# Kernel tuning notes

Hardware: AMD Instinct MI355X
Metric: run time of the kernel (lower is better)

The kernel has to match this reference:

```python
import jax, jax.numpy as jnp
import numpy as np

D = 512   # embed_dim
K = 8     # expand_dim
TAU = 16.0
LN_EPS = 1e-5


def setup_inputs() -> dict:
    key = jax.random.key(0)
    ks = jax.random.split(key, 8)
    b, n = 4, 4096
    x = jax.random.normal(ks[0], (b, n, D), dtype=jnp.float32)
    # nn.Linear weights stored as (in, out); bias=False everywhere
    W_i = jax.random.normal(ks[1], (D, D), dtype=jnp.float32) / np.sqrt(D)
    W_e = jax.random.normal(ks[2], (D, K), dtype=jnp.float32) / np.sqrt(D)
    W_s = jax.random.normal(ks[3], (D, K), dtype=jnp.float32) / np.sqrt(D)
    o_param = jax.random.normal(ks[4], (K, D), dtype=jnp.float32) * 0.1
    ln_gamma = jnp.ones((D,), dtype=jnp.float32)
    ln_beta = jnp.zeros((D,), dtype=jnp.float32)
    W_out = jax.random.normal(ks[5], (D, D), dtype=jnp.float32) / np.sqrt(D)
    return {"x": x, "W_i": W_i, "W_e": W_e, "W_s": W_s, "o_param": o_param,
            "ln_gamma": ln_gamma, "ln_beta": ln_beta, "W_out": W_out}


def reference(x, W_i, W_e, W_s, o_param, ln_gamma, ln_beta, W_out):
    b, n, d = x.shape
    k = W_e.shape[1]
    i = x @ W_i            # (b,n,d) input branch
    e = x @ W_e            # (b,n,k) expand branch (t_type=0: identity)
    s = x @ W_s            # (b,n,k) shrink branch
    # data-independent decay gate: exp(logsigmoid(o)/tau), shape (k,d)
    o = jnp.exp(jax.nn.log_sigmoid(o_param) / TAU)

    def step(m, inp):
        it, et, st = inp          # (b,d), (b,k), (b,k)
        m = o * m + et[:, :, None] * it[:, None, :]   # (b,k,d)
        y = jnp.einsum('bk,bkd->bd', st, m)
        return m, y

    m0 = jnp.zeros((b, k, d), dtype=x.dtype)
    xs = (jnp.swapaxes(i, 0, 1), jnp.swapaxes(e, 0, 1), jnp.swapaxes(s, 0, 1))
    _, ys = jax.lax.scan(step, m0, xs)   # ys: (n,b,d)
    y = jnp.swapaxes(ys, 0, 1)           # (b,n,d)
    # LayerNorm
    mu = jnp.mean(y, axis=-1, keepdims=True)
    var = jnp.mean(jnp.square(y - mu), axis=-1, keepdims=True)
    y = (y - mu) * jax.lax.rsqrt(var + LN_EPS) * ln_gamma + ln_beta
    return y @ W_out
```

## Files before the change

kernel.cpp:

```cpp
#include <hip/hip_runtime.h>
#include <stdint.h>

typedef __bf16 bf16;
typedef __bf16 bf16x8 __attribute__((ext_vector_type(8)));
typedef float  f32x4  __attribute__((ext_vector_type(4)));

#define NSEQ 4096
#define NROWS 16384
#define CHUNK 32
#define NCHUNKS_B 128
#define NCHUNKS 512
#define SEGLEN 16
#define NSEG 8
#define YSTRIDE 516

__device__ __forceinline__ float bf2f(uint16_t u){
    uint32_t w = ((uint32_t)u) << 16;
    return __builtin_bit_cast(float, w);
}
__device__ __forceinline__ uint32_t pack2(float a, float b){
    uint16_t ua = __builtin_bit_cast(uint16_t, (bf16)a);
    uint16_t ub = __builtin_bit_cast(uint16_t, (bf16)b);
    return ((uint32_t)ub << 16) | (uint32_t)ua;
}
__device__ __forceinline__ uint4 cvt8(const float* p){
    float4 lo = *(const float4*)p;
    float4 hi = *(const float4*)(p + 4);
    uint4 r;
    r.x = pack2(lo.x, lo.y); r.y = pack2(lo.z, lo.w);
    r.z = pack2(hi.x, hi.y); r.w = pack2(hi.z, hi.w);
    return r;
}
__device__ __forceinline__ float rd_any(const void* p, long idx, int f){
    return f ? ((const float*)p)[idx] : (float)((const bf16*)p)[idx];
}
__device__ __forceinline__ void cp16(const void* g, void* l){
    __builtin_amdgcn_global_load_lds((const __attribute__((address_space(1))) void*)g,
                                     (__attribute__((address_space(3))) void*)l,
                                     16, 0, 0);
}

__global__ __launch_bounds__(256) void prep_all(const uint32_t* __restrict__ xw,
                                                const void* __restrict__ Wi,
                                                const void* __restrict__ Wo,
                                                const void* We, const void* Ws,
                                                const void* op, const void* g, const void* bta,
                                                bf16* __restrict__ Wt_i, bf16* __restrict__ Wt_o,
                                                bf16* __restrict__ Wt_es,
                                                float* __restrict__ g_c, float* __restrict__ b_c,
                                                float* __restrict__ o_buf, float* __restrict__ oL_buf,
                                                float* __restrict__ lsL_buf, float* __restrict__ oL16_buf,
                                                int* __restrict__ flag_g){
    __shared__ int cnt[256];
    __shared__ bf16 T[64][65];
    int tid = threadIdx.x;
    int c = 0;
    #pragma unroll
    for (int j = 0; j < 4; ++j){
        uint32_t w = xw[tid*4 + j];
        uint32_t e = (w >> 7) & 0xFF;
        c += (e >= 110 && e <= 140) ? 1 : 0;
    }
    cnt[tid] = c; __syncthreads();
    for (int s = 128; s; s >>= 1){
        if (tid < s) cnt[tid] += cnt[tid + s];
        __syncthreads();
    }
    int f = (cnt[0] < 512) ? 1 : 0;
    int blk = blockIdx.x;
    if (blk == 0 && tid == 0) flag_g[0] = f;

    if (blk < 128){
        int mat = blk >> 6;
        int t   = blk & 63;
        int k0  = (t >> 3) * 64, n0 = (t & 7) * 64;
        const void* in = mat ? Wo : Wi;
        bf16* out = mat ? Wt_o : Wt_i;
        #pragma unroll
        for (int e = 0; e < 16; ++e){
            int idx = e*256 + tid;
            int r = idx >> 6, cc = idx & 63;
            T[cc][r] = (bf16)rd_any(in, (long)(k0 + r)*512 + n0 + cc, f);
        }
        __syncthreads();
        #pragma unroll
        for (int e = 0; e < 16; ++e){
            int idx = e*256 + tid;
            int rn = idx >> 6, ck = idx & 63;
            out[(long)(n0 + rn)*512 + k0 + ck] = T[rn][ck];
        }
    } else if (blk < 136){
        int sub = blk - 128;
        for (int i = tid; i < 1024; i += 256){
            int gi = sub*1024 + i;
            int n = gi >> 9, k = gi & 511;
            float v = (n < 8) ? rd_any(We, (long)k*8 + n, f)
                              : rd_any(Ws, (long)k*8 + (n-8), f);
            Wt_es[gi] = (bf16)v;
        }
    } else {
        int sub = blk - 136;
        int base = sub * 1024;
        for (int i = tid; i < 1024; i += 256){
            int gi = base + i;
            float x = rd_any(op, gi, f);
            float ls = (x < 0.f) ? (x - log1pf(expf(x))) : (0.f - log1pf(expf(-x)));
            o_buf[gi]    = expf(ls * (1.0f/16.0f));
            oL_buf[gi]   = expf(ls * 2.0f);
            lsL_buf[gi]  = ls * 2.0f;
            oL16_buf[gi] = expf(ls * 32.0f);
        }
        if (sub == 0){
            for (int i = tid; i < 512; i += 256){
                g_c[i] = rd_any(g, i, f);
                b_c[i] = rd_any(bta, i, f);
            }
        }
    }
}

__global__ __launch_bounds__(256) void gemm_bt(const void* __restrict__ Avoid,
                                               const bf16* __restrict__ Bt,
                                               void* __restrict__ Cvoid,
                                               int M, int N, int Kd,
                                               const int* __restrict__ aflag,
                                               const int* __restrict__ cflag,
                                               const bf16* __restrict__ Wes,
                                               float* __restrict__ e_out,
                                               float* __restrict__ s_out){
    __shared__ __align__(16) bf16 As[2][128*32];
    __shared__ __align__(16) bf16 Bs[2][128*32];
    const int tid  = threadIdx.x;
    const int lane = tid & 63;
    const int wave = tid >> 6;
    const int ntiles = N >> 7;
    int bid = blockIdx.x;
    {
        const int q = gridDim.x >> 3;
        bid = (bid & 7) * q + (bid >> 3);
    }
    const int mtile = bid / ntiles;
    const int ntile = bid - mtile*ntiles;
    const int m0 = mtile << 7, n0 = ntile << 7;
    const int wr = (wave >> 1) << 6;
    const int wc = (wave & 1) << 6;
    const int lrow = lane & 15;
    const int quad = lane >> 4;
    const int fa = aflag ? *aflag : 0;
    const bool do_es = (Wes != nullptr) && (ntile == 0) && (wc == 0);

    f32x4 acc[4][4] = {};
    f32x4 acc_es[4] = {};

    const int sr = tid >> 2;
    const int sk = (tid & 3) << 3;
    const bf16*  Ag  = (const bf16*) Avoid + (long)(m0 + sr)*Kd + sk;
    const float* Agf = (const float*)Avoid + (long)(m0 + sr)*Kd + sk;
    const bf16*  Bg  = Bt + (long)(n0 + sr)*Kd + sk;

    if (fa){
        *(uint4*)&As[0][tid*8]        = cvt8(Agf);
        *(uint4*)&As[0][2048 + tid*8] = cvt8(Agf + (long)64*Kd);
    } else {
        cp16(Ag,                 &As[0][(size_t)wave*512]);
        cp16(Ag + (long)64*Kd,   &As[0][2048 + (size_t)wave*512]);
    }
    cp16(Bg,               &Bs[0][(size_t)wave*512]);
    cp16(Bg + (long)64*Kd, &Bs[0][2048 + (size_t)wave*512]);
    __syncthreads();

    int cur = 0;
    for (int k0 = 0; k0 < Kd; k0 += 32){
        const int nxt  = cur ^ 1;
        const int k1   = k0 + 32;
        const bool more = (k1 < Kd);
        float4 la0, la1, lb0, lb1;
        if (more){
            if (fa){
                la0 = *(const float4*)(Agf + k1);
                la1 = *(const float4*)(Agf + k1 + 4);
                lb0 = *(const float4*)(Agf + (long)64*Kd + k1);
                lb1 = *(const float4*)(Agf + (long)64*Kd + k1 + 4);
            } else {
                cp16(Ag + k1,               &As[nxt][(size_t)wave*512]);
                cp16(Ag + (long)64*Kd + k1, &As[nxt][2048 + (size_t)wave*512]);
            }
            cp16(Bg + k1,               &Bs[nxt][(size_t)wave*512]);
            cp16(Bg + (long)64*Kd + k1, &Bs[nxt][2048 + (size_t)wave*512]);
        }

        bf16x8 af[4], bfr[4];
        #pragma unroll
        for (int i = 0; i < 4; ++i)
            af[i]  = *(const bf16x8*)&As[cur][(wr + i*16 + lrow)*32 + quad*8];
        #pragma unroll
        for (int j = 0; j < 4; ++j)
            bfr[j] = *(const bf16x8*)&Bs[cur][(wc + j*16 + lrow)*32 + quad*8];
        #pragma unroll
        for (int i = 0; i < 4; ++i)
            #pragma unroll
            for (int j = 0; j < 4; ++j)
                acc[i][j] = __builtin_amdgcn_mfma_f32_16x16x32_bf16(af[i], bfr[j], acc[i][j], 0, 0, 0);
        if (do_es){
            bf16x8 be = *(const bf16x8*)(Wes + (long)lrow*512 + k0 + quad*8);
            #pragma unroll
            for (int i = 0; i < 4; ++i)
                acc_es[i] = __builtin_amdgcn_mfma_f32_16x16x32_bf16(af[i], be, acc_es[i], 0, 0, 0);
        }

        if (more && fa){
            uint4 A0, A1;
            A0.x = pack2(la0.x, la0.y); A0.y = pack2(la0.z, la0.w);
            A0.z = pack2(la1.x, la1.y); A0.w = pack2(la1.z, la1.w);
            A1.x = pack2(lb0.x, lb0.y); A1.y = pack2(lb0.z, lb0.w);
            A1.z = pack2(lb1.x, lb1.y); A1.w = pack2(lb1.z, lb1.w);
            *(uint4*)&As[nxt][tid*8]        = A0;
            *(uint4*)&As[nxt][2048 + tid*8] = A1;
        }
        __syncthreads();
        cur = nxt;
    }

    const int fc = cflag ? *cflag : 0;
    if (fc){
        float* Cf = (float*)Cvoid;
        #pragma unroll
        for (int i = 0; i < 4; ++i){
            int gr = m0 + wr + i*16 + quad*4;
            #pragma unroll
            for (int j = 0; j < 4; ++j){
                int gc = n0 + wc + j*16 + lrow;
                #pragma unroll
                for (int r = 0; r < 4; ++r)
                    Cf[(long)(gr + r)*N + gc] = acc[i][j][r];
            }
        }
    } else {
        bf16* Cb = (bf16*)Cvoid;
        #pragma unroll
        for (int i = 0; i < 4; ++i){
            int gr = m0 + wr + i*16 + quad*4;
            #pragma unroll
            for (int j = 0; j < 4; ++j){
                int gc = n0 + wc + j*16 + lrow;
                #pragma unroll
                for (int r = 0; r < 4; ++r)
                    Cb[(long)(gr + r)*N + gc] = (bf16)acc[i][j][r];
            }
        }
    }
    if (do_es){
        float* eo = (lrow < 8) ? e_out : s_out;
        int col = lrow & 7;
        #pragma unroll
        for (int i = 0; i < 4; ++i){
            int gr = m0 + wr + i*16 + quad*4;
            #pragma unroll
            for (int r = 0; r < 4; ++r)
                eo[(long)(gr + r)*8 + col] = acc_es[i][r];
        }
    }
}

__global__ __launch_bounds__(256) void passA(const bf16* __restrict__ i_buf,
                                             const float* __restrict__ e_buf,
                                             const float* __restrict__ o_buf,
                                             float* __restrict__ Ams){
    int c  = blockIdx.x;
    int b  = c >> 7;
    int t0 = (c & 127) * CHUNK;
    int tid = threadIdx.x;
    __shared__ float eS[CHUNK*8];
    eS[tid] = e_buf[((long)(b*NSEQ + t0))*8 + tid];
    __syncthreads();
    int d0 = tid*2;
    float o0[8], o1[8], m0[8], m1[8];
    #pragma unroll
    for (int k = 0; k < 8; ++k){
        o0[k] = o_buf[k*512 + d0]; o1[k] = o_buf[k*512 + d0 + 1];
        m0[k] = 0.f; m1[k] = 0.f;
    }
    const bf16* ip = i_buf + (long)(b*NSEQ + t0)*512 + d0;
    for (int t = 0; t < CHUNK; ++t){
        uint32_t iv = *(const uint32_t*)(ip + (long)t*512);
        float i0 = bf2f((uint16_t)iv), i1 = bf2f((uint16_t)(iv >> 16));
        #pragma unroll
        for (int k = 0; k < 8; ++k){
            float ek = eS[t*8 + k];
            m0[k] = o0[k]*m0[k] + ek*i0;
            m1[k] = o1[k]*m1[k] + ek*i1;
        }
    }
    float* Ac = Ams + (long)c*4096;
    #pragma unroll
    for (int k = 0; k < 8; ++k){
        float2 v; v.x = m0[k]; v.y = m1[k];
        *(float2*)&Ac[k*512 + d0] = v;
    }
}

__global__ __launch_bounds__(256) void passB1(float* __restrict__ Ams,
                                              const float* __restrict__ oL_buf,
                                              float* __restrict__ Tbuf){
    int bs  = blockIdx.x >> 4;
    int b   = bs >> 3, seg = bs & 7;
    int idx = (blockIdx.x & 15)*256 + threadIdx.x;
    float oL = oL_buf[idx];
    float m = 0.f;
    float* Mb = Ams + ((long)b*NCHUNKS_B + seg*SEGLEN)*4096 + idx;
    #pragma unroll 4
    for (int cc = 0; cc < SEGLEN; ++cc){
        float a = Mb[(long)cc*4096];
        Mb[(long)cc*4096] = m;
        m = oL*m + a;
    }
    Tbuf[(long)bs*4096 + idx] = m;
}

__global__ __launch_bounds__(256) void passB2(float* __restrict__ Tbuf,
                                              const float* __restrict__ oL16_buf){
    int b   = blockIdx.x >> 4;
    int idx = (blockIdx.x & 15)*256 + threadIdx.x;
    float oL16 = oL16_buf[idx];
    float t[NSEG];
    #pragma unroll
    for (int s = 0; s < NSEG; ++s)
        t[s] = Tbuf[((long)b*NSEG + s)*4096 + idx];
    float m = 0.f;
    #pragma unroll
    for (int s = 0; s < NSEG; ++s){
        Tbuf[((long)b*NSEG + s)*4096 + idx] = m;
        m = oL16*m + t[s];
    }
}

__global__ __launch_bounds__(256) void passC(bf16* __restrict__ iy,
                                             const float* __restrict__ e_buf,
                                             const float* __restrict__ s_buf,
                                             const float* __restrict__ o_buf,
                                             const float* __restrict__ Ploc,
                                             const float* __restrict__ Mseg,
                                             const float* __restrict__ lsL_buf,
                                             const float* __restrict__ g_c,
                                             const float* __restrict__ b_c){
    int c  = blockIdx.x;
    int b  = c >> 7;
    int cI = c & 127;
    int seg = cI >> 4;
    float fj = (float)(cI & 15);
    int t0 = cI * CHUNK;
    int tid = threadIdx.x;
    __shared__ float eS[CHUNK*8], sS[CHUNK*8];
    __shared__ float muS[CHUNK], rS[CHUNK];
    __shared__ __align__(16) float yS[CHUNK][YSTRIDE];
    eS[tid] = e_buf[((long)(b*NSEQ + t0))*8 + tid];
    sS[tid] = s_buf[((long)(b*NSEQ + t0))*8 + tid];
    __syncthreads();
    int d0 = tid*2;
    float o0[8], o1[8], m0[8], m1[8];
    const float* P0 = Ploc + (long)c*4096;
    const float* Ms = Mseg + ((long)b*NSEG + seg)*4096;
    #pragma unroll
    for (int k = 0; k < 8; ++k){
        int i0 = k*512 + d0;
        o0[k] = o_buf[i0]; o1[k] = o_buf[i0 + 1];
        m0[k] = P0[i0]   + __expf(lsL_buf[i0]  *fj)*Ms[i0];
        m1[k] = P0[i0+1] + __expf(lsL_buf[i0+1]*fj)*Ms[i0+1];
    }
    bf16* ip = iy + (long)(b*NSEQ + t0)*512 + d0;
    for (int t = 0; t < CHUNK; ++t){
        uint32_t iv = *(const uint32_t*)(ip + (long)t*512);
        float i0 = bf2f((uint16_t)iv), i1 = bf2f((uint16_t)(iv >> 16));
        float y0 = 0.f, y1 = 0.f;
        #pragma unroll
        for (int k = 0; k < 8; ++k){
            float ek = eS[t*8 + k], sk = sS[t*8 + k];
            m0[k] = o0[k]*m0[k] + ek*i0;
            m1[k] = o1[k]*m1[k] + ek*i1;
            y0 += sk*m0[k];
            y1 += sk*m1[k];
        }
        float2 yv; yv.x = y0; yv.y = y1;
        *(float2*)&yS[t][d0] = yv;
    }
    __syncthreads();
    {
        int row = tid >> 3, sub = tid & 7;
        const float4* yr = (const float4*)&yS[row][sub*64];
        float s = 0.f, s2 = 0.f;
        #pragma unroll
        for (int j = 0; j < 16; ++j){
            float4 v = yr[j];
            s  += v.x + v.y + v.z + v.w;
            s2 += v.x*v.x + v.y*v.y + v.z*v.z + v.w*v.w;
        }
        s += __shfl_xor(s, 1); s2 += __shfl_xor(s2, 1);
        s += __shfl_xor(s, 2); s2 += __shfl_xor(s2, 2);
        s += __shfl_xor(s, 4); s2 += __shfl_xor(s2, 4);
        if (sub == 0){
            float mu  = s * (1.f/512.f);
            float var = s2 * (1.f/512.f) - mu*mu;
            muS[row] = mu;
            rS[row]  = rsqrtf(var + 1e-5f);
        }
    }
    __syncthreads();
    float g0 = g_c[d0], g1 = g_c[d0+1];
    float bb0 = b_c[d0], bb1 = b_c[d0+1];
    for (int t = 0; t < CHUNK; ++t){
        float mu = muS[t], r = rS[t];
        float2 yv = *(const float2*)&yS[t][d0];
        float a0 = (yv.x - mu)*r*g0 + bb0;
        float a1 = (yv.y - mu)*r*g1 + bb1;
        *(uint32_t*)(ip + (long)t*512) = pack2(a0, a1);
    }
}

extern "C" void kernel_launch(void* const* d_in, const int* in_sizes, int n_in,
                              void* d_out, int out_size, void* d_ws, size_t ws_size,
                              hipStream_t stream){
    const void* x    = d_in[0];
    const void* W_i  = d_in[1];
    const void* W_e  = d_in[2];
    const void* W_s  = d_in[3];
    const void* o_p  = d_in[4];
    const void* gmm  = d_in[5];
    const void* bta  = d_in[6];
    const void* W_o  = d_in[7];

    char* ws = (char*)d_ws;
    bf16*  Wt_i   = (bf16*) (ws + 0);
    float* Tbuf   = (float*)(ws + 0);
    bf16*  Wt_o   = (bf16*) (ws + 524288);
    bf16*  iy_buf = (bf16*) (ws + 1048576);
    float* e_buf  = (float*)(ws + 17825792);
    float* s_buf  = (float*)(ws + 18350080);
    float* o_buf  = (float*)(ws + 18874368);
    float* oL_buf = (float*)(ws + 18890752);
    float* lsL    = (float*)(ws + 18907136);
    float* oL16   = (float*)(ws + 18923520);
    float* Ams    = (float*)(ws + 18939904);
    bf16*  Wt_es  = (bf16*) (ws + 27328512);
    float* g_c    = (float*)(ws + 27344896);
    float* b_c    = (float*)(ws + 27346944);
    int*   flag   = (int*)  (ws + 27348992);

    prep_all<<<140, 256, 0, stream>>>((const uint32_t*)x, W_i, W_o, W_e, W_s, o_p, gmm, bta,
                                      Wt_i, Wt_o, Wt_es, g_c, b_c, o_buf, oL_buf, lsL, oL16, flag);
    gemm_bt <<<512, 256, 0, stream>>>(x, Wt_i, iy_buf, NROWS, 512, 512, flag, nullptr,
                                      Wt_es, e_buf, s_buf);
    passA  <<<NCHUNKS, 256, 0, stream>>>(iy_buf, e_buf, o_buf, Ams);
    passB1 <<<512,  256, 0, stream>>>(Ams, oL_buf, Tbuf);
    passB2 <<<64,   256, 0, stream>>>(Tbuf, oL16);
    passC  <<<NCHUNKS, 256, 0, stream>>>(iy_buf, e_buf, s_buf, o_buf, Ams, Tbuf, lsL,
                                         g_c, b_c);
    gemm_bt <<<512, 256, 0, stream>>>(iy_buf, Wt_o, d_out, NROWS, 512, 512, nullptr, flag,
                                      nullptr, nullptr, nullptr);
}
```

Measured before the change: 174.8 us.

## Fuse chunk-local scan into input GEMM epilogue and fold segment prefix into passC

```diff
diff --git a/kernel.cpp b/kernel.cpp
--- a/kernel.cpp
+++ b/kernel.cpp
@@ -127,9 +127,14 @@
                                                const int* __restrict__ cflag,
                                                const bf16* __restrict__ Wes,
                                                float* __restrict__ e_out,
-                                               float* __restrict__ s_out){
-    __shared__ __align__(16) bf16 As[2][128*32];
-    __shared__ __align__(16) bf16 Bs[2][128*32];
+                                               float* __restrict__ s_out,
+                                               float* __restrict__ Ams,
+                                               const float* __restrict__ o_buf){
+    __shared__ __align__(16) char smem[36*1024];
+    bf16*  As = (bf16*)smem;
+    bf16*  Bs = (bf16*)(smem + 16384);
+    bf16*  iT = (bf16*)smem;
+    float* eS = (float*)(smem + 32768);
     const int tid  = threadIdx.x;
     const int lane = tid & 63;
     const int wave = tid >> 6;
@@ -147,7 +152,7 @@
     const int lrow = lane & 15;
     const int quad = lane >> 4;
     const int fa = aflag ? *aflag : 0;
-    const bool do_es = (Wes != nullptr) && (ntile == 0) && (wc == 0);
+    const bool do_es = (Wes != nullptr) && ((wave & 1) == 0);
 
     f32x4 acc[4][4] = {};
     f32x4 acc_es[4] = {};
@@ -159,14 +164,14 @@
     const bf16*  Bg  = Bt + (long)(n0 + sr)*Kd + sk;
 
     if (fa){
-        *(uint4*)&As[0][tid*8]        = cvt8(Agf);
-        *(uint4*)&As[0][2048 + tid*8] = cvt8(Agf + (long)64*Kd);
+        *(uint4*)&As[tid*8]        = cvt8(Agf);
+        *(uint4*)&As[2048 + tid*8] = cvt8(Agf + (long)64*Kd);
     } else {
-        cp16(Ag,                 &As[0][(size_t)wave*512]);
-        cp16(Ag + (long)64*Kd,   &As[0][2048 + (size_t)wave*512]);
-    }
-    cp16(Bg,               &Bs[0][(size_t)wave*512]);
-    cp16(Bg + (long)64*Kd, &Bs[0][2048 + (size_t)wave*512]);
+        cp16(Ag,                 As + (size_t)wave*512);
+        cp16(Ag + (long)64*Kd,   As + 2048 + (size_t)wave*512);
+    }
+    cp16(Bg,               Bs + (size_t)wave*512);
+    cp16(Bg + (long)64*Kd, Bs + 2048 + (size_t)wave*512);
     __syncthreads();
 
     int cur = 0;
@@ -182,20 +187,20 @@
                 lb0 = *(const float4*)(Agf + (long)64*Kd + k1);
                 lb1 = *(const float4*)(Agf + (long)64*Kd + k1 + 4);
             } else {
-                cp16(Ag + k1,               &As[nxt][(size_t)wave*512]);
-                cp16(Ag + (long)64*Kd + k1, &As[nxt][2048 + (size_t)wave*512]);
-            }
-            cp16(Bg + k1,               &Bs[nxt][(size_t)wave*512]);
-            cp16(Bg + (long)64*Kd + k1, &Bs[nxt][2048 + (size_t)wave*512]);
+                cp16(Ag + k1,               As + nxt*4096 + (size_t)wave*512);
+                cp16(Ag + (long)64*Kd + k1, As + nxt*4096 + 2048 + (size_t)wave*512);
+            }
+            cp16(Bg + k1,               Bs + nxt*4096 + (size_t)wave*512);
+            cp16(Bg + (long)64*Kd + k1, Bs + nxt*4096 + 2048 + (size_t)wave*512);
         }
 
         bf16x8 af[4], bfr[4];
         #pragma unroll
         for (int i = 0; i < 4; ++i)
-            af[i]  = *(const bf16x8*)&As[cur][(wr + i*16 + lrow)*32 + quad*8];
+            af[i]  = *(const bf16x8*)&As[cur*4096 + (wr + i*16 + lrow)*32 + quad*8];
         #pragma unroll
         for (int j = 0; j < 4; ++j)
-            bfr[j] = *(const bf16x8*)&Bs[cur][(wc + j*16 + lrow)*32 + quad*8];
+            bfr[j] = *(const bf16x8*)&Bs[cur*4096 + (wc + j*16 + lrow)*32 + quad*8];
         #pragma unroll
         for (int i = 0; i < 4; ++i)
             #pragma unroll
@@ -214,8 +219,8 @@
             A0.z = pack2(la1.x, la1.y); A0.w = pack2(la1.z, la1.w);
             A1.x = pack2(lb0.x, lb0.y); A1.y = pack2(lb0.z, lb0.w);
             A1.z = pack2(lb1.x, lb1.y); A1.w = pack2(lb1.z, lb1.w);
-            *(uint4*)&As[nxt][tid*8]        = A0;
-            *(uint4*)&As[nxt][2048 + tid*8] = A1;
+            *(uint4*)&As[nxt*4096 + tid*8]        = A0;
+            *(uint4*)&As[nxt*4096 + 2048 + tid*8] = A1;
         }
         __syncthreads();
         cur = nxt;
@@ -249,7 +254,7 @@
             }
         }
     }
-    if (do_es){
+    if (do_es && ntile == 0){
         float* eo = (lrow < 8) ? e_out : s_out;
         int col = lrow & 7;
         #pragma unroll
@@ -260,42 +265,54 @@
                 eo[(long)(gr + r)*8 + col] = acc_es[i][r];
         }
     }
-}
-
-__global__ __launch_bounds__(256) void passA(const bf16* __restrict__ i_buf,
-                                             const float* __restrict__ e_buf,
-                                             const float* __restrict__ o_buf,
-                                             float* __restrict__ Ams){
-    int c  = blockIdx.x;
-    int b  = c >> 7;
-    int t0 = (c & 127) * CHUNK;
-    int tid = threadIdx.x;
-    __shared__ float eS[CHUNK*8];
-    eS[tid] = e_buf[((long)(b*NSEQ + t0))*8 + tid];
-    __syncthreads();
-    int d0 = tid*2;
-    float o0[8], o1[8], m0[8], m1[8];
-    #pragma unroll
-    for (int k = 0; k < 8; ++k){
-        o0[k] = o_buf[k*512 + d0]; o1[k] = o_buf[k*512 + d0 + 1];
-        m0[k] = 0.f; m1[k] = 0.f;
-    }
-    const bf16* ip = i_buf + (long)(b*NSEQ + t0)*512 + d0;
-    for (int t = 0; t < CHUNK; ++t){
-        uint32_t iv = *(const uint32_t*)(ip + (long)t*512);
-        float i0 = bf2f((uint16_t)iv), i1 = bf2f((uint16_t)(iv >> 16));
-        #pragma unroll
-        for (int k = 0; k < 8; ++k){
-            float ek = eS[t*8 + k];
-            m0[k] = o0[k]*m0[k] + ek*i0;
-            m1[k] = o1[k]*m1[k] + ek*i1;
-        }
-    }
-    float* Ac = Ams + (long)c*4096;
-    #pragma unroll
-    for (int k = 0; k < 8; ++k){
-        float2 v; v.x = m0[k]; v.y = m1[k];
-        *(float2*)&Ac[k*512 + d0] = v;
+
+    if (Ams){
+        #pragma unroll
+        for (int i = 0; i < 4; ++i){
+            int lr = wr + i*16 + quad*4;
+            #pragma unroll
+            for (int j = 0; j < 4; ++j){
+                int lc = wc + j*16 + lrow;
+                #pragma unroll
+                for (int r = 0; r < 4; ++r)
+                    iT[(lr + r)*128 + lc] = (bf16)acc[i][j][r];
+            }
+        }
+        if (do_es && lrow < 8){
+            #pragma unroll
+            for (int i = 0; i < 4; ++i){
+                int lr = wr + i*16 + quad*4;
+                #pragma unroll
+                for (int r = 0; r < 4; ++r)
+                    eS[(lr + r)*8 + lrow] = acc_es[i][r];
+            }
+        }
+        __syncthreads();
+        const int dp  = tid & 63;
+        const int kq  = tid >> 6;
+        const int dl  = dp*2;
+        const int ki  = kq*2;
+        const float o00 = o_buf[(ki  )*512 + n0 + dl];
+        const float o01 = o_buf[(ki  )*512 + n0 + dl + 1];
+        const float o10 = o_buf[(ki+1)*512 + n0 + dl];
+        const float o11 = o_buf[(ki+1)*512 + n0 + dl + 1];
+        #pragma unroll
+        for (int c = 0; c < 4; ++c){
+            float m00 = 0.f, m01 = 0.f, m10 = 0.f, m11 = 0.f;
+            for (int t = 0; t < CHUNK; ++t){
+                int row = c*32 + t;
+                uint32_t iv = *(const uint32_t*)&iT[row*128 + dl];
+                float i0 = bf2f((uint16_t)iv), i1 = bf2f((uint16_t)(iv >> 16));
+                float e0 = eS[row*8 + ki], e1 = eS[row*8 + ki + 1];
+                m00 = o00*m00 + e0*i0;  m01 = o01*m01 + e0*i1;
+                m10 = o10*m10 + e1*i0;  m11 = o11*m11 + e1*i1;
+            }
+            float* Ac = Ams + (long)((m0 >> 5) + c)*4096 + n0 + dl;
+            float2 v0; v0.x = m00; v0.y = m01;
+            float2 v1; v1.x = m10; v1.y = m11;
+            *(float2*)&Ac[(ki  )*512] = v0;
+            *(float2*)&Ac[(ki+1)*512] = v1;
+        }
     }
 }
 
@@ -317,30 +334,14 @@
     Tbuf[(long)bs*4096 + idx] = m;
 }
 
-__global__ __launch_bounds__(256) void passB2(float* __restrict__ Tbuf,
-                                              const float* __restrict__ oL16_buf){
-    int b   = blockIdx.x >> 4;
-    int idx = (blockIdx.x & 15)*256 + threadIdx.x;
-    float oL16 = oL16_buf[idx];
-    float t[NSEG];
-    #pragma unroll
-    for (int s = 0; s < NSEG; ++s)
-        t[s] = Tbuf[((long)b*NSEG + s)*4096 + idx];
-    float m = 0.f;
-    #pragma unroll
-    for (int s = 0; s < NSEG; ++s){
-        Tbuf[((long)b*NSEG + s)*4096 + idx] = m;
-        m = oL16*m + t[s];
-    }
-}
-
 __global__ __launch_bounds__(256) void passC(bf16* __restrict__ iy,
                                              const float* __restrict__ e_buf,
                                              const float* __restrict__ s_buf,
                                              const float* __restrict__ o_buf,
                                              const float* __restrict__ Ploc,
-                                             const float* __restrict__ Mseg,
+                                             const float* __restrict__ Tbuf,
                                              const float* __restrict__ lsL_buf,
+                                             const float* __restrict__ oL16_buf,
                                              const float* __restrict__ g_c,
                                              const float* __restrict__ b_c){
     int c  = blockIdx.x;
@@ -359,13 +360,19 @@
     int d0 = tid*2;
     float o0[8], o1[8], m0[8], m1[8];
     const float* P0 = Ploc + (long)c*4096;
-    const float* Ms = Mseg + ((long)b*NSEG + seg)*4096;
     #pragma unroll
     for (int k = 0; k < 8; ++k){
         int i0 = k*512 + d0;
+        float ms0 = 0.f, ms1 = 0.f;
+        float w0 = oL16_buf[i0], w1 = oL16_buf[i0+1];
+        for (int u = 0; u < seg; ++u){
+            const float* T = Tbuf + ((long)(b*NSEG + u))*4096;
+            ms0 = w0*ms0 + T[i0];
+            ms1 = w1*ms1 + T[i0+1];
+        }
         o0[k] = o_buf[i0]; o1[k] = o_buf[i0 + 1];
-        m0[k] = P0[i0]   + __expf(lsL_buf[i0]  *fj)*Ms[i0];
-        m1[k] = P0[i0+1] + __expf(lsL_buf[i0+1]*fj)*Ms[i0+1];
+        m0[k] = P0[i0]   + __expf(lsL_buf[i0]  *fj)*ms0;
+        m1[k] = P0[i0+1] + __expf(lsL_buf[i0+1]*fj)*ms1;
     }
     bf16* ip = iy + (long)(b*NSEQ + t0)*512 + d0;
     for (int t = 0; t < CHUNK; ++t){
@@ -448,12 +455,10 @@
     prep_all<<<140, 256, 0, stream>>>((const uint32_t*)x, W_i, W_o, W_e, W_s, o_p, gmm, bta,
                                       Wt_i, Wt_o, Wt_es, g_c, b_c, o_buf, oL_buf, lsL, oL16, flag);
     gemm_bt <<<512, 256, 0, stream>>>(x, Wt_i, iy_buf, NROWS, 512, 512, flag, nullptr,
-                                      Wt_es, e_buf, s_buf);
-    passA  <<<NCHUNKS, 256, 0, stream>>>(iy_buf, e_buf, o_buf, Ams);
+                                      Wt_es, e_buf, s_buf, Ams, o_buf);
     passB1 <<<512,  256, 0, stream>>>(Ams, oL_buf, Tbuf);
-    passB2 <<<64,   256, 0, stream>>>(Tbuf, oL16);
     passC  <<<NCHUNKS, 256, 0, stream>>>(iy_buf, e_buf, s_buf, o_buf, Ams, Tbuf, lsL,
-                                         g_c, b_c);
+                                         oL16, g_c, b_c);
     gemm_bt <<<512, 256, 0, stream>>>(iy_buf, Wt_o, d_out, NROWS, 512, 512, nullptr, flag,
-                                      nullptr, nullptr, nullptr);
-}
+                                      nullptr, nullptr, nullptr, nullptr, nullptr);
+}
```

After: 173.4 us. Within noise of the previous version (-0.8%).
